# Kernel tuning notes

Measured on AMD Instinct MI355X. Metric: run time of the kernel, lower is better.

Reference implementation:

```python
import jax, jax.numpy as jnp
import numpy as np

B, L, V, H, NL = 128, 512, 2048, 512, 2


def setup_inputs() -> dict:
    key = jax.random.key(0)
    ks = jax.random.split(key, 20)
    s = 0.05  # param scale
    inp = {
        "input_ids": jax.random.randint(ks[0], (B,), 0, V),
        "last_hidden": jax.random.normal(ks[1], (NL, B, H), jnp.float32),
        "word_dict_vec": jax.random.normal(ks[2], (B, V, H), jnp.float32),
        "encoder_outputs": jax.random.normal(ks[3], (L, B, H), jnp.float32),
        "seq_mask": (jax.random.uniform(ks[4], (B, L)) < 0.2).at[:, 0].set(False),
        # Attn params (torch Linear: y = x @ W.T + b)
        "attn_W": jax.random.normal(ks[5], (H, 2 * H), jnp.float32) * s,
        "attn_b": jax.random.normal(ks[6], (H,), jnp.float32) * s,
        "score_W": jax.random.normal(ks[7], (1, H), jnp.float32) * s,
        # concat layer
        "concat_W": jax.random.normal(ks[8], (H, 2 * H), jnp.float32) * s,
        "concat_b": jax.random.normal(ks[9], (H,), jnp.float32) * s,
        # GRU layer 0 (input 2H) and layer 1 (input H); gates ordered r,z,n as in torch
        "W_ih0": jax.random.normal(ks[10], (3 * H, 2 * H), jnp.float32) * s,
        "W_hh0": jax.random.normal(ks[11], (3 * H, H), jnp.float32) * s,
        "b_ih0": jax.random.normal(ks[12], (3 * H,), jnp.float32) * s,
        "b_hh0": jax.random.normal(ks[13], (3 * H,), jnp.float32) * s,
        "W_ih1": jax.random.normal(ks[14], (3 * H, H), jnp.float32) * s,
        "W_hh1": jax.random.normal(ks[15], (3 * H, H), jnp.float32) * s,
        "b_ih1": jax.random.normal(ks[16], (3 * H,), jnp.float32) * s,
        "b_hh1": jax.random.normal(ks[17], (3 * H,), jnp.float32) * s,
    }
    return inp


def _gru_cell(x, h, W_ih, W_hh, b_ih, b_hh):
    gi = x @ W_ih.T + b_ih
    gh = h @ W_hh.T + b_hh
    i_r, i_z, i_n = jnp.split(gi, 3, axis=-1)
    h_r, h_z, h_n = jnp.split(gh, 3, axis=-1)
    r = jax.nn.sigmoid(i_r + h_r)
    z = jax.nn.sigmoid(i_z + h_z)
    n = jnp.tanh(i_n + r * h_n)
    return (1.0 - z) * n + z * h


def reference(input_ids, last_hidden, word_dict_vec, encoder_outputs, seq_mask,
              attn_W, attn_b, score_W, concat_W, concat_b,
              W_ih0, W_hh0, b_ih0, b_hh0, W_ih1, W_hh1, b_ih1, b_hh1):
    # one_hot @ word_dict_vec == per-batch row gather (same math)
    emb = word_dict_vec[jnp.arange(B), input_ids]  # [B, H]

    # Bahdanau additive attention over encoder_outputs [L, B, H]
    q = last_hidden[-1]  # [B, H]
    hid = jnp.broadcast_to(q[None], (L, B, H))
    energy_in = jnp.concatenate([hid, encoder_outputs], axis=2)  # [L, B, 2H]
    e = jnp.tanh(energy_in @ attn_W.T + attn_b) @ score_W.T      # [L, B, 1]
    scores = e[..., 0].T                                          # [B, L]
    scores = jnp.where(seq_mask, jnp.float32(-1e12), scores)
    aw = jax.nn.softmax(scores, axis=1)                           # [B, L]

    context = jnp.einsum('bl,lbh->bh', aw, encoder_outputs)       # [B, H]

    # single-step 2-layer GRU (eval mode: dropout = identity)
    x0 = jnp.concatenate([emb, context], axis=1)                  # [B, 2H]
    h0 = _gru_cell(x0, last_hidden[0], W_ih0, W_hh0, b_ih0, b_hh0)
    h1 = _gru_cell(h0, last_hidden[1], W_ih1, W_hh1, b_ih1, b_hh1)
    hidden = jnp.stack([h0, h1])                                  # [2, B, H]

    output = jnp.tanh(jnp.concatenate([h1, context], axis=1) @ concat_W.T + concat_b)
    return output, hidden
```

## Files before the change

### kernel.cpp

```cpp
#include <hip/hip_runtime.h>
#include <stdint.h>

#define Hdim 512
#define Bdim 128
#define Ldim 512
#define Vdim 2048

typedef unsigned short u16;
using f32x4  = float  __attribute__((ext_vector_type(4)));
using f32x8  = float  __attribute__((ext_vector_type(8)));
using bf16x8 = __bf16 __attribute__((ext_vector_type(8)));
using bf16x2 = __bf16 __attribute__((ext_vector_type(2)));

__device__ inline u16 f2bf(float x) {
  __bf16 b = (__bf16)x;
  union { __bf16 b; u16 u; } c; c.b = b; return c.u;
}
__device__ inline uint32_t pk2(float lo, float hi) {
  union { bf16x2 v; uint32_t u; } c;
  c.v[0] = (__bf16)lo; c.v[1] = (__bf16)hi;
  return c.u;
}
__device__ inline float fast_tanh(float x) {
  return 1.0f - 2.0f / (__expf(2.0f * x) + 1.0f);
}
__device__ inline float fast_sig(float x) { return 1.0f / (1.0f + __expf(-x)); }

__device__ inline bf16x8 pack_bf8(float4 x, float4 y) {
  f32x8 f = {x.x, x.y, x.z, x.w, y.x, y.y, y.z, y.w};
  return __builtin_convertvector(f, bf16x8);
}

__global__ __launch_bounds__(512)
void prep_kernel(const float* __restrict__ lh, const float* __restrict__ attn_W,
                 const float* __restrict__ attn_b, const float* __restrict__ cat_W,
                 const float* __restrict__ W_ih0, const float* __restrict__ W_hh0,
                 const float* __restrict__ W_ih1, const float* __restrict__ W_hh1,
                 const float* __restrict__ b_ih0, const float* __restrict__ b_hh0,
                 const float* __restrict__ b_ih1, const float* __restrict__ b_hh1,
                 const float* __restrict__ wdv, const int* __restrict__ ids,
                 const void* __restrict__ mask,
                 float* __restrict__ qW, u16* __restrict__ arena,
                 float* __restrict__ biasg0, float* __restrict__ biasg1,
                 u16* __restrict__ X0bf, u16* __restrict__ X1bf, int* __restrict__ flag) {
  int blk = blockIdx.x, t = threadIdx.x;
  int lane = t & 63, wid = t >> 6;
  int fr = lane & 15, g = lane >> 4, kof = g * 8;

  if (blk < 16) {
    int mh = wid & 3, nh = wid >> 2;
    int n0 = blk * 32 + nh * 16;
    int rb0 = mh * 32;
    f32x4 ac0 = {0.f, 0.f, 0.f, 0.f}, ac1 = {0.f, 0.f, 0.f, 0.f};
    const float* q = lh + 65536;
#pragma unroll 2
    for (int kt = 0; kt < 512; kt += 32) {
      const float* qr0 = q + (size_t)(rb0 + fr) * 512 + kt + kof;
      const float* qr1 = qr0 + 16 * 512;
      const float* wr  = attn_W + (size_t)(n0 + fr) * 1024 + kt + kof;
      float4 x0 = *(const float4*)qr0, x1 = *(const float4*)(qr0 + 4);
      float4 y0 = *(const float4*)qr1, y1 = *(const float4*)(qr1 + 4);
      float4 w0 = *(const float4*)wr,  w1 = *(const float4*)(wr + 4);
      bf16x8 A0 = pack_bf8(x0, x1), A1 = pack_bf8(y0, y1), Bb = pack_bf8(w0, w1);
      ac0 = __builtin_amdgcn_mfma_f32_16x16x32_bf16(A0, Bb, ac0, 0, 0, 0);
      ac1 = __builtin_amdgcn_mfma_f32_16x16x32_bf16(A1, Bb, ac1, 0, 0, 0);
    }
    float vb = attn_b[n0 + fr];
#pragma unroll
    for (int j = 0; j < 4; ++j) {
      qW[(size_t)(rb0 + g * 4 + j) * 512 + n0 + fr]      = ac0[j] + vb;
      qW[(size_t)(rb0 + 16 + g * 4 + j) * 512 + n0 + fr] = ac1[j] + vb;
    }
    return;
  }
  if (blk == 16) {
    __shared__ int sf;
    if (t == 0) sf = 0;
    __syncthreads();
    const uint32_t* m32 = (const uint32_t*)mask;
    int found = 0;
    for (int i = t; i < 16384; i += 512)
      if (m32[i] & 0xffffff00u) found = 1;
    if (found) sf = 1;
    __syncthreads();
    if (t == 0) *flag = sf;
    return;
  }
  const int ARENA_Q = 1507328;
  int i = (blk - 17) * 512 + t;
  if (i < ARENA_Q) {
    int e = i * 4;
    float4 v = {0.f, 0.f, 0.f, 0.f};
    if (e < 262144) {
      int o = e >> 9, k = e & 511;
      v = *(const float4*)(attn_W + (size_t)o * 1024 + 512 + k);
    } else if (e < 786432) {
      int e2 = e - 262144; int o = e2 >> 10, k = e2 & 1023;
      v = *(const float4*)(cat_W + (size_t)o * 1024 + k);
    } else if (e < 3932160) {
      int e2 = e - 786432; int row = e2 / 1536, k = e2 % 1536;
      int o = row >> 2, gt = row & 3;
      if (gt == 0)      v = (k < 1024) ? *(const float4*)(W_ih0 + (size_t)o * 1024 + k)
                                       : *(const float4*)(W_hh0 + (size_t)o * 512 + k - 1024);
      else if (gt == 1) v = (k < 1024) ? *(const float4*)(W_ih0 + (size_t)(512 + o) * 1024 + k)
                                       : *(const float4*)(W_hh0 + (size_t)(512 + o) * 512 + k - 1024);
      else if (gt == 2) { if (k < 1024)  v = *(const float4*)(W_ih0 + (size_t)(1024 + o) * 1024 + k); }
      else              { if (k >= 1024) v = *(const float4*)(W_hh0 + (size_t)(1024 + o) * 512 + k - 1024); }
    } else {
      int e2 = e - 3932160; int row = e2 >> 10, k = e2 & 1023;
      int o = row >> 2, gt = row & 3;
      if (gt == 0)      v = (k < 512) ? *(const float4*)(W_ih1 + (size_t)o * 512 + k)
                                      : *(const float4*)(W_hh1 + (size_t)o * 512 + k - 512);
      else if (gt == 1) v = (k < 512) ? *(const float4*)(W_ih1 + (size_t)(512 + o) * 512 + k)
                                      : *(const float4*)(W_hh1 + (size_t)(512 + o) * 512 + k - 512);
      else if (gt == 2) { if (k < 512)  v = *(const float4*)(W_ih1 + (size_t)(1024 + o) * 512 + k); }
      else              { if (k >= 512) v = *(const float4*)(W_hh1 + (size_t)(1024 + o) * 512 + k - 512); }
    }
    ushort4 u;
    u.x = f2bf(v.x); u.y = f2bf(v.y); u.z = f2bf(v.z); u.w = f2bf(v.w);
    *(ushort4*)(arena + e) = u;
    return;
  }
  int i2 = i - ARENA_Q;
  if (i2 < 1024) {
    int r4 = i2 * 4; int layer = r4 >> 11; int r = r4 & 2047; int o = r >> 2;
    const float* bi = layer ? b_ih1 : b_ih0;
    const float* bh = layer ? b_hh1 : b_hh0;
    float4 v;
    v.x = bi[o] + bh[o];
    v.y = bi[512 + o] + bh[512 + o];
    v.z = bi[1024 + o];
    v.w = bh[1024 + o];
    *(float4*)((layer ? biasg1 : biasg0) + r) = v;
  } else if (i2 < 1024 + 16384) {
    int j = (i2 - 1024) * 4; int b = j >> 9, i0 = j & 511;
    float4 v = *(const float4*)(wdv + (size_t)b * (Vdim * Hdim) + (size_t)ids[b] * 512 + i0);
    ushort4 u;
    u.x = f2bf(v.x); u.y = f2bf(v.y); u.z = f2bf(v.z); u.w = f2bf(v.w);
    *(ushort4*)(X0bf + b * 1536 + i0) = u;
  } else if (i2 < 1024 + 32768) {
    int j = (i2 - 1024 - 16384) * 4; int b = j >> 9, i0 = j & 511;
    float4 v = *(const float4*)(lh + (size_t)b * 512 + i0);
    ushort4 u;
    u.x = f2bf(v.x); u.y = f2bf(v.y); u.z = f2bf(v.z); u.w = f2bf(v.w);
    *(ushort4*)(X0bf + b * 1536 + 1024 + i0) = u;
  } else if (i2 < 1024 + 49152) {
    int j = (i2 - 1024 - 32768) * 4; int b = j >> 9, i0 = j & 511;
    float4 v = *(const float4*)(lh + 65536 + (size_t)b * 512 + i0);
    ushort4 u;
    u.x = f2bf(v.x); u.y = f2bf(v.y); u.z = f2bf(v.z); u.w = f2bf(v.w);
    *(ushort4*)(X1bf + b * 1024 + 512 + i0) = u;
  }
}

__global__ __launch_bounds__(512)
void attn_kernel(const float* __restrict__ enc, const u16* __restrict__ Wenc,
                 const float* __restrict__ qW, const float* __restrict__ scW,
                 float* __restrict__ scores_p) {
  __shared__ __align__(16) u16 As[2][128 * 40];
  __shared__ float part[8 * 128];
  int blk = blockIdx.x, t = threadIdx.x;
  int lane = t & 63, wid = t >> 6;
  int fr = lane & 15, g = lane >> 4, kof = g * 8;
  int l  = (blk >> 4) * 8 + (blk & 7);
  int oh = (blk >> 3) & 1;
  int ob = oh * 256;
  const int arow = t >> 2;
  const int aks = (t & 3) * 8;

  f32x4 acc[8][2];
#pragma unroll
  for (int i = 0; i < 8; ++i) {
    acc[i][0] = (f32x4){0.f, 0.f, 0.f, 0.f};
    acc[i][1] = (f32x4){0.f, 0.f, 0.f, 0.f};
  }
  const float* abase = enc + ((size_t)l * 128 + arow) * 512 + aks;
  const u16* bptr0 = Wenc + (size_t)(ob + wid * 32 + fr) * 512 + kof;
  const u16* bptr1 = bptr0 + (size_t)16 * 512;

  float4 pA0 = *(const float4*)abase;
  float4 pA1 = *(const float4*)(abase + 4);
  float4 pB0 = *(const float4*)(abase + 32);
  float4 pB1 = *(const float4*)(abase + 36);
  bf16x8 cb0 = *(const bf16x8*)bptr0;
  bf16x8 cb1 = *(const bf16x8*)bptr1;

#pragma unroll 2
  for (int step = 0; step < 16; ++step) {
    int sel = step & 1;
    __syncthreads();
    bf16x8 apv = pack_bf8(pA0, pA1);
    *(bf16x8*)(&As[sel][arow * 40 + aks]) = apv;
    pA0 = pB0; pA1 = pB1;
    if (step < 14) {
      int kt = (step + 2) * 32;
      pB0 = *(const float4*)(abase + kt);
      pB1 = *(const float4*)(abase + kt + 4);
    }
    bf16x8 nb0 = cb0, nb1 = cb1;
    if (step < 15) {
      int kt = (step + 1) * 32;
      nb0 = *(const bf16x8*)(bptr0 + kt);
      nb1 = *(const bf16x8*)(bptr1 + kt);
    }
    __syncthreads();
#pragma unroll
    for (int mi = 0; mi < 8; ++mi) {
      bf16x8 av = *(const bf16x8*)(&As[sel][(mi * 16 + fr) * 40 + kof]);
      acc[mi][0] = __builtin_amdgcn_mfma_f32_16x16x32_bf16(av, cb0, acc[mi][0], 0, 0, 0);
      acc[mi][1] = __builtin_amdgcn_mfma_f32_16x16x32_bf16(av, cb1, acc[mi][1], 0, 0, 0);
    }
    cb0 = nb0; cb1 = nb1;
  }
#pragma unroll
  for (int mi = 0; mi < 8; ++mi) {
    float rs0 = 0.f, rs1 = 0.f, rs2 = 0.f, rs3 = 0.f;
#pragma unroll
    for (int ni = 0; ni < 2; ++ni) {
      int o = ob + wid * 32 + ni * 16 + fr;
      float sw = scW[o];
      int brow = mi * 16 + g * 4;
      rs0 += sw * fast_tanh(acc[mi][ni][0] + qW[(size_t)(brow + 0) * 512 + o]);
      rs1 += sw * fast_tanh(acc[mi][ni][1] + qW[(size_t)(brow + 1) * 512 + o]);
      rs2 += sw * fast_tanh(acc[mi][ni][2] + qW[(size_t)(brow + 2) * 512 + o]);
      rs3 += sw * fast_tanh(acc[mi][ni][3] + qW[(size_t)(brow + 3) * 512 + o]);
    }
#pragma unroll
    for (int d = 1; d < 16; d <<= 1) {
      rs0 += __shfl_xor(rs0, d);
      rs1 += __shfl_xor(rs1, d);
      rs2 += __shfl_xor(rs2, d);
      rs3 += __shfl_xor(rs3, d);
    }
    if (fr < 4) {
      float v = (fr == 0) ? rs0 : (fr == 1) ? rs1 : (fr == 2) ? rs2 : rs3;
      part[wid * 128 + mi * 16 + g * 4 + fr] = v;
    }
  }
  __syncthreads();
  if (t < 128) {
    float s = 0.f;
#pragma unroll
    for (int w2 = 0; w2 < 8; ++w2) s += part[w2 * 128 + t];
    scores_p[(size_t)(oh * 128 + t) * 512 + l] = s;
  }
}

__global__ __launch_bounds__(256)
void softctx_kernel(const float* __restrict__ sp, const void* __restrict__ maskp,
                    const int* __restrict__ flag, const float* __restrict__ enc,
                    u16* __restrict__ X0bf, u16* __restrict__ c1bf) {
  __shared__ float wgt[512];
  __shared__ float redm[4], reds[4];
  __shared__ float ps[256 * 2];
  int blk = blockIdx.x, t = threadIdx.x;
  int lane = t & 63, wid = t >> 6;
  int b = blk >> 4, c = blk & 15;
  int l0 = t, l1 = t + 256;
  float s0 = sp[(size_t)b * 512 + l0] + sp[(size_t)(128 + b) * 512 + l0];
  float s1 = sp[(size_t)b * 512 + l1] + sp[(size_t)(128 + b) * 512 + l1];
  bool isbyte = (*flag != 0);
  bool m0, m1;
  if (isbyte) {
    m0 = ((const uint8_t*)maskp)[b * 512 + l0] != 0;
    m1 = ((const uint8_t*)maskp)[b * 512 + l1] != 0;
  } else {
    m0 = ((const int*)maskp)[b * 512 + l0] != 0;
    m1 = ((const int*)maskp)[b * 512 + l1] != 0;
  }
  float v0 = m0 ? -1e12f : s0;
  float v1 = m1 ? -1e12f : s1;
  float mx = fmaxf(v0, v1);
#pragma unroll
  for (int d = 1; d < 64; d <<= 1) mx = fmaxf(mx, __shfl_xor(mx, d));
  if (lane == 0) redm[wid] = mx;
  __syncthreads();
  mx = fmaxf(fmaxf(redm[0], redm[1]), fmaxf(redm[2], redm[3]));
  float e0 = __expf(v0 - mx), e1 = __expf(v1 - mx);
  float sm = e0 + e1;
#pragma unroll
  for (int d = 1; d < 64; d <<= 1) sm += __shfl_xor(sm, d);
  if (lane == 0) reds[wid] = sm;
  __syncthreads();
  sm = reds[0] + reds[1] + reds[2] + reds[3];
  float inv = 1.0f / sm;
  wgt[l0] = e0 * inv;
  wgt[l1] = e1 * inv;
  __syncthreads();
  int cp = t & 15, lq = t >> 4;
  int col = c * 32 + cp * 2;
  float a0 = 0.f, a1 = 0.f;
  const float* ebase = enc + (size_t)b * 512 + col;
#pragma unroll 4
  for (int l2 = lq * 32; l2 < lq * 32 + 32; ++l2) {
    float wl = wgt[l2];
    float2 ev = *(const float2*)(ebase + (size_t)l2 * 65536);
    a0 += wl * ev.x;
    a1 += wl * ev.y;
  }
  ps[(lq * 16 + cp) * 2 + 0] = a0;
  ps[(lq * 16 + cp) * 2 + 1] = a1;
  __syncthreads();
  if (t < 16) {
    float r0 = 0.f, r1 = 0.f;
#pragma unroll
    for (int q2 = 0; q2 < 16; ++q2) {
      r0 += ps[(q2 * 16 + t) * 2 + 0];
      r1 += ps[(q2 * 16 + t) * 2 + 1];
    }
    int cc = c * 32 + t * 2;
    uint32_t packed = pk2(r0, r1);
    *(uint32_t*)(X0bf + b * 1536 + 512 + cc) = packed;
    *(uint32_t*)(c1bf + b * 1024 + 512 + cc) = packed;
  }
}

__global__ __launch_bounds__(256)
void gru_gemm_kernel(const u16* __restrict__ X, int ldx, const u16* __restrict__ Wp,
                     const float* __restrict__ biasp, const float* __restrict__ hprev,
                     int K, float* __restrict__ hout, u16* __restrict__ xdst) {
  __shared__ float ct[128][36];
  int n0 = blockIdx.x * 32;
  int t = threadIdx.x, lane = t & 63, w = t >> 6;
  int fr = lane & 15, g = lane >> 4, kof = g * 8;
  f32x4 acc[2][2];
#pragma unroll
  for (int i = 0; i < 2; ++i)
#pragma unroll
    for (int j = 0; j < 2; ++j) acc[i][j] = (f32x4){0.f, 0.f, 0.f, 0.f};
  const u16* Xr0 = X + (size_t)(w * 32 + fr) * ldx;
  const u16* Xr1 = Xr0 + (size_t)16 * ldx;
  const u16* Wr0 = Wp + (size_t)(n0 + fr) * K;
  const u16* Wr1 = Wp + (size_t)(n0 + 16 + fr) * K;
#pragma unroll 4
  for (int kt = 0; kt < K; kt += 32) {
    bf16x8 a0 = *(const bf16x8*)(Xr0 + kt + kof);
    bf16x8 a1 = *(const bf16x8*)(Xr1 + kt + kof);
    bf16x8 b0 = *(const bf16x8*)(Wr0 + kt + kof);
    bf16x8 b1 = *(const bf16x8*)(Wr1 + kt + kof);
    acc[0][0] = __builtin_amdgcn_mfma_f32_16x16x32_bf16(a0, b0, acc[0][0], 0, 0, 0);
    acc[0][1] = __builtin_amdgcn_mfma_f32_16x16x32_bf16(a0, b1, acc[0][1], 0, 0, 0);
    acc[1][0] = __builtin_amdgcn_mfma_f32_16x16x32_bf16(a1, b0, acc[1][0], 0, 0, 0);
    acc[1][1] = __builtin_amdgcn_mfma_f32_16x16x32_bf16(a1, b1, acc[1][1], 0, 0, 0);
  }
#pragma unroll
  for (int mi = 0; mi < 2; ++mi)
#pragma unroll
    for (int ni = 0; ni < 2; ++ni) {
      int col = ni * 16 + fr;
      float vb = biasp[n0 + col];
#pragma unroll
      for (int j = 0; j < 4; ++j)
        ct[w * 32 + 16 * mi + g * 4 + j][col] = acc[mi][ni][j] + vb;
    }
  __syncthreads();
#pragma unroll
  for (int i = 0; i < 4; ++i) {
    int u = t + i * 256;
    int b = u >> 3, ol = u & 7;
    float cr  = ct[b][ol * 4 + 0];
    float cz  = ct[b][ol * 4 + 1];
    float ci  = ct[b][ol * 4 + 2];
    float chh = ct[b][ol * 4 + 3];
    int o = blockIdx.x * 8 + ol;
    float r = fast_sig(cr), z = fast_sig(cz);
    float n = tanhf(ci + r * chh);
    float h = (1.0f - z) * n + z * hprev[b * 512 + o];
    hout[b * 512 + o] = h;
    xdst[b * 1024 + o] = f2bf(h);
  }
}

__global__ __launch_bounds__(256)
void thin_gemm32(const u16* __restrict__ X, int ldx, const u16* __restrict__ W,
                 const float* __restrict__ bias, float* __restrict__ C, int ldc,
                 int K, int act) {
  int n0 = blockIdx.x * 32;
  int t = threadIdx.x, lane = t & 63, w = t >> 6;
  int fr = lane & 15, g = lane >> 4, kof = g * 8;
  f32x4 acc[2][2];
#pragma unroll
  for (int i = 0; i < 2; ++i)
#pragma unroll
    for (int j = 0; j < 2; ++j) acc[i][j] = (f32x4){0.f, 0.f, 0.f, 0.f};
  const u16* Xr0 = X + (size_t)(w * 32 + fr) * ldx;
  const u16* Xr1 = Xr0 + (size_t)16 * ldx;
  const u16* Wr0 = W + (size_t)(n0 + fr) * K;
  const u16* Wr1 = W + (size_t)(n0 + 16 + fr) * K;
#pragma unroll 4
  for (int kt = 0; kt < K; kt += 32) {
    bf16x8 a0 = *(const bf16x8*)(Xr0 + kt + kof);
    bf16x8 a1 = *(const bf16x8*)(Xr1 + kt + kof);
    bf16x8 b0 = *(const bf16x8*)(Wr0 + kt + kof);
    bf16x8 b1 = *(const bf16x8*)(Wr1 + kt + kof);
    acc[0][0] = __builtin_amdgcn_mfma_f32_16x16x32_bf16(a0, b0, acc[0][0], 0, 0, 0);
    acc[0][1] = __builtin_amdgcn_mfma_f32_16x16x32_bf16(a0, b1, acc[0][1], 0, 0, 0);
    acc[1][0] = __builtin_amdgcn_mfma_f32_16x16x32_bf16(a1, b0, acc[1][0], 0, 0, 0);
    acc[1][1] = __builtin_amdgcn_mfma_f32_16x16x32_bf16(a1, b1, acc[1][1], 0, 0, 0);
  }
#pragma unroll
  for (int mi = 0; mi < 2; ++mi)
#pragma unroll
    for (int ni = 0; ni < 2; ++ni) {
      int col = n0 + ni * 16 + fr;
      float vb = bias[col];
#pragma unroll
      for (int j = 0; j < 4; ++j) {
        int row = w * 32 + 16 * mi + g * 4 + j;
        float v = acc[mi][ni][j] + vb;
        if (act) v = tanhf(v);
        C[(size_t)row * ldc + col] = v;
      }
    }
}

extern "C" void kernel_launch(void* const* d_in, const int* in_sizes, int n_in,
                              void* d_out, int out_size, void* d_ws, size_t ws_size,
                              hipStream_t stream) {
  const int*   ids    = (const int*)  d_in[0];
  const float* lh     = (const float*)d_in[1];
  const float* wdv    = (const float*)d_in[2];
  const float* enc    = (const float*)d_in[3];
  const void*  mask   = d_in[4];
  const float* attn_W = (const float*)d_in[5];
  const float* attn_b = (const float*)d_in[6];
  const float* scW    = (const float*)d_in[7];
  const float* cat_W  = (const float*)d_in[8];
  const float* cat_b  = (const float*)d_in[9];
  const float* W_ih0  = (const float*)d_in[10];
  const float* W_hh0  = (const float*)d_in[11];
  const float* b_ih0  = (const float*)d_in[12];
  const float* b_hh0  = (const float*)d_in[13];
  const float* W_ih1  = (const float*)d_in[14];
  const float* W_hh1  = (const float*)d_in[15];
  const float* b_ih1  = (const float*)d_in[16];
  const float* b_hh1  = (const float*)d_in[17];

  float* out = (float*)d_out;
  float* h0  = out + 65536;
  float* h1  = out + 131072;

  float* ws       = (float*)d_ws;
  float* qW       = ws;
  float* scores_p = ws + 65536;
  float* biasg0   = ws + 196608;
  float* biasg1   = ws + 198656;
  int*   flag     = (int*)(ws + 200704);
  u16*   arena    = (u16*)(ws + 200720);
  u16*   X0bf     = (u16*)(ws + 3215376);
  u16*   X1bf     = (u16*)(ws + 3313680);
  u16*   c1bf     = (u16*)(ws + 3379216);

  const u16* Wenc = arena;
  const u16* Wcat = arena + 262144;
  const u16* Wg0p = arena + 786432;
  const u16* Wg1p = arena + 3932160;

  prep_kernel<<<3059, 512, 0, stream>>>(lh, attn_W, attn_b, cat_W,
                                        W_ih0, W_hh0, W_ih1, W_hh1,
                                        b_ih0, b_hh0, b_ih1, b_hh1,
                                        wdv, ids, mask,
                                        qW, arena, biasg0, biasg1, X0bf, X1bf, flag);
  attn_kernel<<<1024, 512, 0, stream>>>(enc, Wenc, qW, scW, scores_p);
  softctx_kernel<<<2048, 256, 0, stream>>>(scores_p, mask, flag, enc, X0bf, c1bf);
  gru_gemm_kernel<<<64, 256, 0, stream>>>(X0bf, 1536, Wg0p, biasg0, lh, 1536, h0, X1bf);
  gru_gemm_kernel<<<64, 256, 0, stream>>>(X1bf, 1024, Wg1p, biasg1, lh + 65536, 1024, h1, c1bf);
  thin_gemm32<<<16, 256, 0, stream>>>(c1bf, 1024, Wcat, cat_b, out, 512, 1024, 1);
}
```

Before: 172.6 us.

## Fuse attention scoring with split-softmax context and finalize partial chunks

Result: slower. 198.1 us (+14.8%).

```diff
diff --git a/kernel.cpp b/kernel.cpp
--- a/kernel.cpp
+++ b/kernel.cpp
@@ -154,165 +154,160 @@
 }
 
 __global__ __launch_bounds__(512)
-void attn_kernel(const float* __restrict__ enc, const u16* __restrict__ Wenc,
-                 const float* __restrict__ qW, const float* __restrict__ scW,
-                 float* __restrict__ scores_p) {
+void attn_fused_kernel(const float* __restrict__ enc, const u16* __restrict__ Wenc,
+                       const float* __restrict__ qW, const float* __restrict__ scW,
+                       const void* __restrict__ maskp, const int* __restrict__ flag,
+                       float* __restrict__ ctxp, float* __restrict__ ms) {
   __shared__ __align__(16) u16 As[2][128 * 40];
   __shared__ float part[8 * 128];
+  __shared__ float score[128];
+  __shared__ float redx[8];
   int blk = blockIdx.x, t = threadIdx.x;
   int lane = t & 63, wid = t >> 6;
   int fr = lane & 15, g = lane >> 4, kof = g * 8;
-  int l  = (blk >> 4) * 8 + (blk & 7);
-  int oh = (blk >> 3) & 1;
-  int ob = oh * 256;
+  int b = blk >> 2, lc = blk & 3;
   const int arow = t >> 2;
   const int aks = (t & 3) * 8;
 
-  f32x4 acc[8][2];
-#pragma unroll
-  for (int i = 0; i < 8; ++i) {
-    acc[i][0] = (f32x4){0.f, 0.f, 0.f, 0.f};
-    acc[i][1] = (f32x4){0.f, 0.f, 0.f, 0.f};
-  }
-  const float* abase = enc + ((size_t)l * 128 + arow) * 512 + aks;
-  const u16* bptr0 = Wenc + (size_t)(ob + wid * 32 + fr) * 512 + kof;
-  const u16* bptr1 = bptr0 + (size_t)16 * 512;
-
-  float4 pA0 = *(const float4*)abase;
-  float4 pA1 = *(const float4*)(abase + 4);
-  float4 pB0 = *(const float4*)(abase + 32);
-  float4 pB1 = *(const float4*)(abase + 36);
-  bf16x8 cb0 = *(const bf16x8*)bptr0;
-  bf16x8 cb1 = *(const bf16x8*)bptr1;
+  if (t < 128) score[t] = 0.f;
+
+  const float* abase = enc + (((size_t)(lc * 128 + arow)) * 128 + b) * 512 + aks;
+
+  for (int oh = 0; oh < 2; ++oh) {
+    int ob = oh * 256;
+    f32x4 acc[8][2];
+#pragma unroll
+    for (int i = 0; i < 8; ++i) {
+      acc[i][0] = (f32x4){0.f, 0.f, 0.f, 0.f};
+      acc[i][1] = (f32x4){0.f, 0.f, 0.f, 0.f};
+    }
+    const u16* bptr0 = Wenc + (size_t)(ob + wid * 32 + fr) * 512 + kof;
+    const u16* bptr1 = bptr0 + (size_t)16 * 512;
+    float4 pA0 = *(const float4*)abase;
+    float4 pA1 = *(const float4*)(abase + 4);
+    float4 pB0 = *(const float4*)(abase + 32);
+    float4 pB1 = *(const float4*)(abase + 36);
+    bf16x8 cb0 = *(const bf16x8*)bptr0;
+    bf16x8 cb1 = *(const bf16x8*)bptr1;
 
 #pragma unroll 2
-  for (int step = 0; step < 16; ++step) {
-    int sel = step & 1;
+    for (int step = 0; step < 16; ++step) {
+      int sel = step & 1;
+      __syncthreads();
+      bf16x8 apv = pack_bf8(pA0, pA1);
+      *(bf16x8*)(&As[sel][arow * 40 + aks]) = apv;
+      pA0 = pB0; pA1 = pB1;
+      if (step < 14) {
+        int kt = (step + 2) * 32;
+        pB0 = *(const float4*)(abase + kt);
+        pB1 = *(const float4*)(abase + kt + 4);
+      }
+      bf16x8 nb0 = cb0, nb1 = cb1;
+      if (step < 15) {
+        int kt = (step + 1) * 32;
+        nb0 = *(const bf16x8*)(bptr0 + kt);
+        nb1 = *(const bf16x8*)(bptr1 + kt);
+      }
+      __syncthreads();
+#pragma unroll
+      for (int mi = 0; mi < 8; ++mi) {
+        bf16x8 av = *(const bf16x8*)(&As[sel][(mi * 16 + fr) * 40 + kof]);
+        acc[mi][0] = __builtin_amdgcn_mfma_f32_16x16x32_bf16(av, cb0, acc[mi][0], 0, 0, 0);
+        acc[mi][1] = __builtin_amdgcn_mfma_f32_16x16x32_bf16(av, cb1, acc[mi][1], 0, 0, 0);
+      }
+      cb0 = nb0; cb1 = nb1;
+    }
+    float sw0 = scW[ob + wid * 32 + fr];
+    float sw1 = scW[ob + wid * 32 + 16 + fr];
+    float q0  = qW[(size_t)b * 512 + ob + wid * 32 + fr];
+    float q1  = qW[(size_t)b * 512 + ob + wid * 32 + 16 + fr];
+#pragma unroll
+    for (int mi = 0; mi < 8; ++mi) {
+      float rs0 = sw0 * fast_tanh(acc[mi][0][0] + q0) + sw1 * fast_tanh(acc[mi][1][0] + q1);
+      float rs1 = sw0 * fast_tanh(acc[mi][0][1] + q0) + sw1 * fast_tanh(acc[mi][1][1] + q1);
+      float rs2 = sw0 * fast_tanh(acc[mi][0][2] + q0) + sw1 * fast_tanh(acc[mi][1][2] + q1);
+      float rs3 = sw0 * fast_tanh(acc[mi][0][3] + q0) + sw1 * fast_tanh(acc[mi][1][3] + q1);
+#pragma unroll
+      for (int d = 1; d < 16; d <<= 1) {
+        rs0 += __shfl_xor(rs0, d);
+        rs1 += __shfl_xor(rs1, d);
+        rs2 += __shfl_xor(rs2, d);
+        rs3 += __shfl_xor(rs3, d);
+      }
+      if (fr < 4) {
+        float v = (fr == 0) ? rs0 : (fr == 1) ? rs1 : (fr == 2) ? rs2 : rs3;
+        part[wid * 128 + mi * 16 + g * 4 + fr] = v;
+      }
+    }
     __syncthreads();
-    bf16x8 apv = pack_bf8(pA0, pA1);
-    *(bf16x8*)(&As[sel][arow * 40 + aks]) = apv;
-    pA0 = pB0; pA1 = pB1;
-    if (step < 14) {
-      int kt = (step + 2) * 32;
-      pB0 = *(const float4*)(abase + kt);
-      pB1 = *(const float4*)(abase + kt + 4);
-    }
-    bf16x8 nb0 = cb0, nb1 = cb1;
-    if (step < 15) {
-      int kt = (step + 1) * 32;
-      nb0 = *(const bf16x8*)(bptr0 + kt);
-      nb1 = *(const bf16x8*)(bptr1 + kt);
+    if (t < 128) {
+      float s = 0.f;
+#pragma unroll
+      for (int w2 = 0; w2 < 8; ++w2) s += part[w2 * 128 + t];
+      score[t] += s;
     }
     __syncthreads();
-#pragma unroll
-    for (int mi = 0; mi < 8; ++mi) {
-      bf16x8 av = *(const bf16x8*)(&As[sel][(mi * 16 + fr) * 40 + kof]);
-      acc[mi][0] = __builtin_amdgcn_mfma_f32_16x16x32_bf16(av, cb0, acc[mi][0], 0, 0, 0);
-      acc[mi][1] = __builtin_amdgcn_mfma_f32_16x16x32_bf16(av, cb1, acc[mi][1], 0, 0, 0);
-    }
-    cb0 = nb0; cb1 = nb1;
-  }
-#pragma unroll
-  for (int mi = 0; mi < 8; ++mi) {
-    float rs0 = 0.f, rs1 = 0.f, rs2 = 0.f, rs3 = 0.f;
-#pragma unroll
-    for (int ni = 0; ni < 2; ++ni) {
-      int o = ob + wid * 32 + ni * 16 + fr;
-      float sw = scW[o];
-      int brow = mi * 16 + g * 4;
-      rs0 += sw * fast_tanh(acc[mi][ni][0] + qW[(size_t)(brow + 0) * 512 + o]);
-      rs1 += sw * fast_tanh(acc[mi][ni][1] + qW[(size_t)(brow + 1) * 512 + o]);
-      rs2 += sw * fast_tanh(acc[mi][ni][2] + qW[(size_t)(brow + 2) * 512 + o]);
-      rs3 += sw * fast_tanh(acc[mi][ni][3] + qW[(size_t)(brow + 3) * 512 + o]);
-    }
-#pragma unroll
-    for (int d = 1; d < 16; d <<= 1) {
-      rs0 += __shfl_xor(rs0, d);
-      rs1 += __shfl_xor(rs1, d);
-      rs2 += __shfl_xor(rs2, d);
-      rs3 += __shfl_xor(rs3, d);
-    }
-    if (fr < 4) {
-      float v = (fr == 0) ? rs0 : (fr == 1) ? rs1 : (fr == 2) ? rs2 : rs3;
-      part[wid * 128 + mi * 16 + g * 4 + fr] = v;
-    }
+  }
+
+  bool isbyte = (*flag != 0);
+  if (t < 128) {
+    int l = lc * 128 + t;
+    bool m = isbyte ? (((const uint8_t*)maskp)[b * 512 + l] != 0)
+                    : (((const int*)maskp)[b * 512 + l] != 0);
+    if (m) score[t] = -1e12f;
   }
   __syncthreads();
+  float v = (t < 128) ? score[t] : -1e12f;
+#pragma unroll
+  for (int d = 1; d < 64; d <<= 1) v = fmaxf(v, __shfl_xor(v, d));
+  if (lane == 0) redx[wid] = v;
+  __syncthreads();
+  float mloc = redx[0];
+#pragma unroll
+  for (int w2 = 1; w2 < 8; ++w2) mloc = fmaxf(mloc, redx[w2]);
+  float e = 0.f;
   if (t < 128) {
-    float s = 0.f;
-#pragma unroll
-    for (int w2 = 0; w2 < 8; ++w2) s += part[w2 * 128 + t];
-    scores_p[(size_t)(oh * 128 + t) * 512 + l] = s;
-  }
-}
-
-__global__ __launch_bounds__(256)
-void softctx_kernel(const float* __restrict__ sp, const void* __restrict__ maskp,
-                    const int* __restrict__ flag, const float* __restrict__ enc,
-                    u16* __restrict__ X0bf, u16* __restrict__ c1bf) {
-  __shared__ float wgt[512];
-  __shared__ float redm[4], reds[4];
-  __shared__ float ps[256 * 2];
-  int blk = blockIdx.x, t = threadIdx.x;
-  int lane = t & 63, wid = t >> 6;
-  int b = blk >> 4, c = blk & 15;
-  int l0 = t, l1 = t + 256;
-  float s0 = sp[(size_t)b * 512 + l0] + sp[(size_t)(128 + b) * 512 + l0];
-  float s1 = sp[(size_t)b * 512 + l1] + sp[(size_t)(128 + b) * 512 + l1];
-  bool isbyte = (*flag != 0);
-  bool m0, m1;
-  if (isbyte) {
-    m0 = ((const uint8_t*)maskp)[b * 512 + l0] != 0;
-    m1 = ((const uint8_t*)maskp)[b * 512 + l1] != 0;
-  } else {
-    m0 = ((const int*)maskp)[b * 512 + l0] != 0;
-    m1 = ((const int*)maskp)[b * 512 + l1] != 0;
-  }
-  float v0 = m0 ? -1e12f : s0;
-  float v1 = m1 ? -1e12f : s1;
-  float mx = fmaxf(v0, v1);
-#pragma unroll
-  for (int d = 1; d < 64; d <<= 1) mx = fmaxf(mx, __shfl_xor(mx, d));
-  if (lane == 0) redm[wid] = mx;
+    e = __expf(score[t] - mloc);
+  }
   __syncthreads();
-  mx = fmaxf(fmaxf(redm[0], redm[1]), fmaxf(redm[2], redm[3]));
-  float e0 = __expf(v0 - mx), e1 = __expf(v1 - mx);
-  float sm = e0 + e1;
-#pragma unroll
-  for (int d = 1; d < 64; d <<= 1) sm += __shfl_xor(sm, d);
-  if (lane == 0) reds[wid] = sm;
+  if (t < 128) score[t] = e;
+#pragma unroll
+  for (int d = 1; d < 64; d <<= 1) e += __shfl_xor(e, d);
+  if (lane == 0) redx[wid] = e;
   __syncthreads();
-  sm = reds[0] + reds[1] + reds[2] + reds[3];
-  float inv = 1.0f / sm;
-  wgt[l0] = e0 * inv;
-  wgt[l1] = e1 * inv;
-  __syncthreads();
-  int cp = t & 15, lq = t >> 4;
-  int col = c * 32 + cp * 2;
-  float a0 = 0.f, a1 = 0.f;
-  const float* ebase = enc + (size_t)b * 512 + col;
+  float sloc = redx[0] + redx[1] + redx[2] + redx[3] +
+               redx[4] + redx[5] + redx[6] + redx[7];
+  float a = 0.f;
+  const float* eb = enc + (((size_t)(lc * 128)) * 128 + b) * 512 + t;
 #pragma unroll 4
-  for (int l2 = lq * 32; l2 < lq * 32 + 32; ++l2) {
-    float wl = wgt[l2];
-    float2 ev = *(const float2*)(ebase + (size_t)l2 * 65536);
-    a0 += wl * ev.x;
-    a1 += wl * ev.y;
-  }
-  ps[(lq * 16 + cp) * 2 + 0] = a0;
-  ps[(lq * 16 + cp) * 2 + 1] = a1;
-  __syncthreads();
-  if (t < 16) {
-    float r0 = 0.f, r1 = 0.f;
-#pragma unroll
-    for (int q2 = 0; q2 < 16; ++q2) {
-      r0 += ps[(q2 * 16 + t) * 2 + 0];
-      r1 += ps[(q2 * 16 + t) * 2 + 1];
-    }
-    int cc = c * 32 + t * 2;
-    uint32_t packed = pk2(r0, r1);
-    *(uint32_t*)(X0bf + b * 1536 + 512 + cc) = packed;
-    *(uint32_t*)(c1bf + b * 1024 + 512 + cc) = packed;
-  }
+  for (int i = 0; i < 128; ++i)
+    a += score[i] * eb[(size_t)i * 65536];
+  ctxp[((size_t)b * 4 + lc) * 512 + t] = a;
+  if (t == 0) {
+    ms[(b * 4 + lc) * 2 + 0] = mloc;
+    ms[(b * 4 + lc) * 2 + 1] = sloc;
+  }
+}
+
+__global__ __launch_bounds__(512)
+void finalize_kernel(const float* __restrict__ ctxp, const float* __restrict__ ms,
+                     u16* __restrict__ X0bf, u16* __restrict__ c1bf) {
+  int b = blockIdx.x, t = threadIdx.x;
+  float m0 = ms[b * 8 + 0], s0 = ms[b * 8 + 1];
+  float m1 = ms[b * 8 + 2], s1 = ms[b * 8 + 3];
+  float m2 = ms[b * 8 + 4], s2 = ms[b * 8 + 5];
+  float m3 = ms[b * 8 + 6], s3 = ms[b * 8 + 7];
+  float M = fmaxf(fmaxf(m0, m1), fmaxf(m2, m3));
+  float e0 = __expf(m0 - M), e1 = __expf(m1 - M);
+  float e2 = __expf(m2 - M), e3 = __expf(m3 - M);
+  float S = s0 * e0 + s1 * e1 + s2 * e2 + s3 * e3;
+  float a = ctxp[((size_t)b * 4 + 0) * 512 + t] * e0
+          + ctxp[((size_t)b * 4 + 1) * 512 + t] * e1
+          + ctxp[((size_t)b * 4 + 2) * 512 + t] * e2
+          + ctxp[((size_t)b * 4 + 3) * 512 + t] * e3;
+  u16 cv = f2bf(a / S);
+  X0bf[b * 1536 + 512 + t] = cv;
+  c1bf[b * 1024 + 512 + t] = cv;
 }
 
 __global__ __launch_bounds__(256)
@@ -440,16 +435,17 @@
   float* h0  = out + 65536;
   float* h1  = out + 131072;
 
-  float* ws       = (float*)d_ws;
-  float* qW       = ws;
-  float* scores_p = ws + 65536;
-  float* biasg0   = ws + 196608;
-  float* biasg1   = ws + 198656;
-  int*   flag     = (int*)(ws + 200704);
-  u16*   arena    = (u16*)(ws + 200720);
-  u16*   X0bf     = (u16*)(ws + 3215376);
-  u16*   X1bf     = (u16*)(ws + 3313680);
-  u16*   c1bf     = (u16*)(ws + 3379216);
+  float* ws     = (float*)d_ws;
+  float* qW     = ws;
+  float* ctxp   = ws + 65536;
+  float* ms     = ws + 327680;
+  float* biasg0 = ws + 328704;
+  float* biasg1 = ws + 330752;
+  int*   flag   = (int*)(ws + 332800);
+  u16*   arena  = (u16*)(ws + 332816);
+  u16*   X0bf   = (u16*)(ws + 3347472);
+  u16*   X1bf   = (u16*)(ws + 3445776);
+  u16*   c1bf   = (u16*)(ws + 3511312);
 
   const u16* Wenc = arena;
   const u16* Wcat = arena + 262144;
@@ -461,8 +457,8 @@
                                         b_ih0, b_hh0, b_ih1, b_hh1,
                                         wdv, ids, mask,
                                         qW, arena, biasg0, biasg1, X0bf, X1bf, flag);
-  attn_kernel<<<1024, 512, 0, stream>>>(enc, Wenc, qW, scW, scores_p);
-  softctx_kernel<<<2048, 256, 0, stream>>>(scores_p, mask, flag, enc, X0bf, c1bf);
+  attn_fused_kernel<<<512, 512, 0, stream>>>(enc, Wenc, qW, scW, mask, flag, ctxp, ms);
+  finalize_kernel<<<128, 512, 0, stream>>>(ctxp, ms, X0bf, c1bf);
   gru_gemm_kernel<<<64, 256, 0, stream>>>(X0bf, 1536, Wg0p, biasg0, lh, 1536, h0, X1bf);
   gru_gemm_kernel<<<64, 256, 0, stream>>>(X1bf, 1024, Wg1p, biasg1, lh + 65536, 1024, h1, c1bf);
   thin_gemm32<<<16, 256, 0, stream>>>(c1bf, 1024, Wcat, cat_b, out, 512, 1024, 1);
```
